# Optimization experiments

Hardware: AMD Instinct MI355X
Metric: run time of the kernel (lower is better)

## Reference

```python
import jax, jax.numpy as jnp
import numpy as np

B, T, F = 512, 1024, 8
H1, H2 = 70, 21   # '80k' config, bidirectional
D1, D2 = 30, 20


def _u(key, shape, fan):
    s = 1.0 / np.sqrt(fan)
    return jax.random.uniform(key, shape, jnp.float32, -s, s)


def setup_inputs() -> dict:
    key = jax.random.key(0)
    ks = iter(jax.random.split(key, 32))
    inp = {"x": jax.random.normal(next(ks), (B, T, F), jnp.float32)}
    # LSTM layer 1 (input F -> H1), forward and backward directions; torch gate order i,f,g,o
    for d in ("f", "b"):
        inp[f"w_ih1_{d}"] = _u(next(ks), (4 * H1, F), H1)
        inp[f"w_hh1_{d}"] = _u(next(ks), (4 * H1, H1), H1)
        inp[f"b_ih1_{d}"] = _u(next(ks), (4 * H1,), H1)
        inp[f"b_hh1_{d}"] = _u(next(ks), (4 * H1,), H1)
    # LSTM layer 2 (input 2*H1 -> H2)
    for d in ("f", "b"):
        inp[f"w_ih2_{d}"] = _u(next(ks), (4 * H2, 2 * H1), H2)
        inp[f"w_hh2_{d}"] = _u(next(ks), (4 * H2, H2), H2)
        inp[f"b_ih2_{d}"] = _u(next(ks), (4 * H2,), H2)
        inp[f"b_hh2_{d}"] = _u(next(ks), (4 * H2,), H2)
    # Dense head: 2*H2 -> D1 -> D2 -> 1
    inp["d1_w"] = _u(next(ks), (D1, 2 * H2), 2 * H2)
    inp["d1_b"] = _u(next(ks), (D1,), 2 * H2)
    inp["d2_w"] = _u(next(ks), (D2, D1), D1)
    inp["d2_b"] = _u(next(ks), (D2,), D1)
    inp["out_w"] = _u(next(ks), (1, D2), D2)
    inp["out_b"] = _u(next(ks), (1,), D2)
    return inp


def _lstm_dir(x, w_ih, w_hh, b_ih, b_hh, reverse):
    # x: [B, T, Fin]; torch LSTM gate order: i, f, g, o
    if reverse:
        x = x[:, ::-1]
    H = w_hh.shape[1]
    pre = jnp.einsum('btf,gf->btg', x, w_ih) + b_ih + b_hh  # [B, T, 4H]
    pre_t = jnp.moveaxis(pre, 1, 0)                          # [T, B, 4H]

    def step(carry, p):
        h, c = carry
        g = p + h @ w_hh.T
        i, f, gg, o = jnp.split(g, 4, axis=-1)
        c = jax.nn.sigmoid(f) * c + jax.nn.sigmoid(i) * jnp.tanh(gg)
        h = jax.nn.sigmoid(o) * jnp.tanh(c)
        return (h, c), h

    init = (jnp.zeros((x.shape[0], H), x.dtype), jnp.zeros((x.shape[0], H), x.dtype))
    _, hs = jax.lax.scan(step, init, pre_t)
    hs = jnp.moveaxis(hs, 0, 1)  # [B, T, H]
    if reverse:
        hs = hs[:, ::-1]
    return hs


def _bilstm(x, wf, uf, bif, bhf, wb, ub, bib, bhb):
    return jnp.concatenate([
        _lstm_dir(x, wf, uf, bif, bhf, reverse=False),
        _lstm_dir(x, wb, ub, bib, bhb, reverse=True),
    ], axis=-1)


def reference(x,
              w_ih1_f, w_hh1_f, b_ih1_f, b_hh1_f,
              w_ih1_b, w_hh1_b, b_ih1_b, b_hh1_b,
              w_ih2_f, w_hh2_f, b_ih2_f, b_hh2_f,
              w_ih2_b, w_hh2_b, b_ih2_b, b_hh2_b,
              d1_w, d1_b, d2_w, d2_b, out_w, out_b):
    h = _bilstm(x, w_ih1_f, w_hh1_f, b_ih1_f, b_hh1_f,
                w_ih1_b, w_hh1_b, b_ih1_b, b_hh1_b)   # [B, T, 2*H1]
    h = _bilstm(h, w_ih2_f, w_hh2_f, b_ih2_f, b_hh2_f,
                w_ih2_b, w_hh2_b, b_ih2_b, b_hh2_b)   # [B, T, 2*H2]
    h = jax.nn.relu(h @ d1_w.T + d1_b)
    h = jax.nn.relu(h @ d2_w.T + d2_b)
    return h @ out_w.T + out_b                          # [B, T, 1]
```

## Files before the change

### kernel.cpp

```cpp
#include <hip/hip_runtime.h>


typedef _Float16 v2f16 __attribute__((ext_vector_type(2)));
typedef _Float16 v4h   __attribute__((ext_vector_type(4)));
typedef _Float16 v8h   __attribute__((ext_vector_type(8)));
typedef float    f32x4 __attribute__((ext_vector_type(4)));

__device__ __forceinline__ float fdot2(v2f16 a, v2f16 b, float c) {
  return __builtin_amdgcn_fdot2(a, b, c, false);
}
#if __has_builtin(__builtin_amdgcn_rcpf)
__device__ __forceinline__ float rcpf(float x) { return __builtin_amdgcn_rcpf(x); }
#else
__device__ __forceinline__ float rcpf(float x) { return 1.f / x; }
#endif
__device__ __forceinline__ float ex2(float v) {
#if __has_builtin(__builtin_amdgcn_exp2f)
  return __builtin_amdgcn_exp2f(v);
#else
  return __expf(v * 0.6931471805599453f);
#endif
}

__device__ __forceinline__ void lds_barrier() {
  asm volatile("s_waitcnt lgkmcnt(0)" ::: "memory");
  __builtin_amdgcn_s_barrier();
  __builtin_amdgcn_sched_barrier(0);
}

#define O_W1M  0u
#define O_WP2  110592u
#define O_W2M  118656u
#define O_BIAS 177792u
#define O_DATA 178496u

__global__ void pack_kernel(const float* __restrict__ wihf, const float* __restrict__ whhf,
                            const float* __restrict__ wihb, const float* __restrict__ whhb,
                            const float* __restrict__ b1if, const float* __restrict__ b1hf,
                            const float* __restrict__ b1ib, const float* __restrict__ b1hb,
                            const float* __restrict__ wih2f, const float* __restrict__ wih2b,
                            const float* __restrict__ whh2f, const float* __restrict__ whh2b,
                            const float* __restrict__ bif, const float* __restrict__ bhf,
                            const float* __restrict__ bib, const float* __restrict__ bhb,
                            char* __restrict__ ws) {
  _Float16* w1m = (_Float16*)(ws + O_W1M);
  _Float16* wp2 = (_Float16*)(ws + O_WP2);
  _Float16* w2m = (_Float16*)(ws + O_W2M);
  float* biasc = (float*)(ws + O_BIAS);
  int idx = blockIdx.x * 256 + threadIdx.x;
  if (idx < 55296) {
    int d = idx / 27648, rem = idx % 27648, rp = rem / 96, k = rem % 96;
    int u = rp >> 2, g = rp & 3;
    const float* wih = d ? wihb : wihf;
    const float* whh = d ? whhb : whhf;
    const float* bi = d ? b1ib : b1if;
    const float* bh = d ? b1hb : b1hf;
    float v = 0.f;
    if (u < 70) {
      int src = g * 70 + u;
      float scale = (g == 2) ? 2.8853900817779268f : 1.4426950408889634f;
      if (k < 8) v = wih[src * 8 + k] * scale;
      else if (k < 78) v = whh[src * 70 + (k - 8)] * scale;
      else if (k == 78) v = (bi[src] + bh[src]) * scale;
    }
    w1m[idx] = (_Float16)v;
  } else if (idx < 59328) {
    int j = idx - 55296;
    int d = j / 2016, rem = j % 2016, r = rem / 24, k = rem % 24;
    const float* whh = d ? whh2b : whh2f;
    wp2[j] = (_Float16)((k < 21) ? whh[r * 21 + k] : 0.f);
  } else if (idx < 88896) {
    int j = idx - 59328;
    int n = j / 168, k = j % 168;
    float v = 0.f;
    if (k < 140) {
      if (n < 84) v = wih2f[n * 140 + k];
      else if (n < 168) v = wih2b[(n - 84) * 140 + k];
    }
    w2m[j] = (_Float16)v;
  } else if (idx < 89072) {
    int n = idx - 88896;
    float v = 0.f;
    if (n < 84) v = bif[n] + bhf[n];
    else if (n < 168) v = bib[n - 84] + bhb[n - 84];
    biasc[n] = v;
  }
}

__global__ __launch_bounds__(768) void lstm1_kernel(
    const float* __restrict__ x,
    const _Float16* __restrict__ w1m,
    _Float16* __restrict__ h1, int b0, int nb) {
  __shared__ __align__(16) _Float16 km[2][16][104];
  const int tid = threadIdx.x;
  const int w = tid >> 6, lane = tid & 63;
  const int q = lane >> 4, bc = lane & 15;
  const int d = blockIdx.y;
  const int blg = blockIdx.x * 16;
  const int gb0 = b0 + blg;

  for (int i = tid; i < 2 * 16 * 104; i += 768) ((_Float16*)km)[i] = (_Float16)0.f;

  int nt, T0;
  if (w < 4)       { nt = 1; T0 = w; }
  else if (w < 10) { nt = 2; T0 = 4 + 2 * (w - 4); }
  else             { nt = 1; T0 = 16 + (w - 10); }

  v8h af[2][3];
#pragma unroll
  for (int i = 0; i < 2; ++i) {
    if (i < nt) {
      int T = T0 + i;
#pragma unroll
      for (int kc = 0; kc < 3; ++kc)
        af[i][kc] = *(const v8h*)&w1m[(size_t)(d * 288 + T * 16 + bc) * 96 + kc * 32 + q * 8];
    }
  }

  __syncthreads();

  if (tid < 16) {
    km[0][tid][78] = (_Float16)1.f;
    km[1][tid][78] = (_Float16)1.f;
  }
  if (tid < 32) {
    int b = tid >> 1, half = tid & 1;
    int t0 = d ? 1023 : 0;
    float4 xv = *(const float4*)&x[((size_t)(gb0 + b) * 1024 + t0) * 8 + half * 4];
    v4h xh; xh[0] = (_Float16)xv.x; xh[1] = (_Float16)xv.y;
    xh[2] = (_Float16)xv.z; xh[3] = (_Float16)xv.w;
    *(v4h*)&km[0][b][half * 4] = xh;
  }
  float c0 = 0.f, c1 = 0.f;
  __syncthreads();

#pragma unroll 1
  for (int s = 0; s < 1024; ++s) {
    const int cur = s & 1, nxt = cur ^ 1;
    float4 xv;
    const bool xl = (tid < 32) && (s < 1023);
    if (xl) {
      int tn = d ? (1022 - s) : (s + 1);
      xv = *(const float4*)&x[((size_t)(gb0 + (tid >> 1)) * 1024 + tn) * 8 + (tid & 1) * 4];
    }
    v8h bf0 = *(const v8h*)&km[cur][bc][q * 8];
    v8h bf1 = *(const v8h*)&km[cur][bc][32 + q * 8];
    v8h bf2 = *(const v8h*)&km[cur][bc][64 + q * 8];
    f32x4 z4 = (f32x4){0.f, 0.f, 0.f, 0.f};
    f32x4 A0 = __builtin_amdgcn_mfma_f32_16x16x32_f16(af[0][0], bf0, z4, 0, 0, 0);
    f32x4 A1 = z4;
    if (nt == 2) A1 = __builtin_amdgcn_mfma_f32_16x16x32_f16(af[1][0], bf0, z4, 0, 0, 0);
    A0 = __builtin_amdgcn_mfma_f32_16x16x32_f16(af[0][1], bf1, A0, 0, 0, 0);
    if (nt == 2) A1 = __builtin_amdgcn_mfma_f32_16x16x32_f16(af[1][1], bf1, A1, 0, 0, 0);
    A0 = __builtin_amdgcn_mfma_f32_16x16x32_f16(af[0][2], bf2, A0, 0, 0, 0);
    if (nt == 2) A1 = __builtin_amdgcn_mfma_f32_16x16x32_f16(af[1][2], bf2, A1, 0, 0, 0);
    const int te = d ? (1023 - s) : s;
    const size_t rowb = ((size_t)te * nb + blg + bc) * 176 + d * 70;

#define GATE(Ai, ci, U)                                                      \
    {                                                                        \
      float ei = ex2(-Ai[0]);                                                \
      float ef = ex2(-Ai[1]);                                                \
      float eg = ex2(-Ai[2]);                                                \
      float eo = ex2(-Ai[3]);                                                \
      float si = rcpf(1.f + ei);                                             \
      float sf = rcpf(1.f + ef);                                             \
      float tg = fmaf(2.f, rcpf(1.f + eg), -1.f);                            \
      float so = rcpf(1.f + eo);                                             \
      ci = fmaf(sf, ci, si * tg);                                            \
      float ec = ex2(ci * -2.8853900817779268f);                             \
      float hv = so * fmaf(2.f, rcpf(1.f + ec), -1.f);                       \
      if ((U) < 70) {                                                        \
        _Float16 hh = (_Float16)hv;                                          \
        km[nxt][bc][8 + (U)] = hh;                                           \
        h1[rowb + (U)] = hh;                                                 \
      }                                                                      \
    }
    GATE(A0, c0, T0 * 4 + q)
    if (nt == 2) GATE(A1, c1, (T0 + 1) * 4 + q)
#undef GATE
    if (xl) {
      v4h xh; xh[0] = (_Float16)xv.x; xh[1] = (_Float16)xv.y;
      xh[2] = (_Float16)xv.z; xh[3] = (_Float16)xv.w;
      *(v4h*)&km[nxt][tid >> 1][(tid & 1) * 4] = xh;
    }
    lds_barrier();
  }
}

__global__ __launch_bounds__(256) void pre2_kernel(
    _Float16* __restrict__ h1, const char* __restrict__ ws) {
  const _Float16* w2m = (const _Float16*)(ws + O_W2M);
  const float* biasc = (const float*)(ws + O_BIAS);
  __shared__ _Float16 Al[64][184];
  __shared__ float Bl[176];
  const int tid = threadIdx.x;
  const int r0 = blockIdx.x * 64;
#pragma unroll
  for (int i = 0; i < 6; ++i) {
    int cid = i * 256 + tid;
    if (cid < 1408) {
      int row = cid / 22, ch = cid % 22;
      *(v8h*)&Al[row][ch * 8] = *(const v8h*)&h1[(size_t)(r0 + row) * 176 + ch * 8];
    }
  }
  if (tid < 176) Bl[tid] = biasc[tid];
  __syncthreads();

  const int wv = tid >> 6, lane = tid & 63;
  const int ml = lane & 15, kq = lane >> 4;
  v8h af[5];
#pragma unroll
  for (int k = 0; k < 4; ++k)
    af[k] = *(const v8h*)&Al[wv * 16 + ml][k * 32 + kq * 8];
  {
    v8h a4 = *(const v8h*)&Al[wv * 16 + ml][128 + kq * 8];
    if (kq >= 2) {
#pragma unroll
      for (int j = 0; j < 8; ++j) a4[j] = (_Float16)0.f;
    } else if (kq == 1) {
#pragma unroll
      for (int j = 4; j < 8; ++j) a4[j] = (_Float16)0.f;
    }
    af[4] = a4;
  }

  const v8h* wg = (const v8h*)w2m;
  f32x4 acc[11];
#pragma unroll
  for (int ct = 0; ct < 11; ++ct) acc[ct] = (f32x4){0.f, 0.f, 0.f, 0.f};

  v8h bc[5], bn[5];
#pragma unroll
  for (int k = 0; k < 5; ++k) bn[k] = wg[(size_t)ml * 21 + k * 4 + kq];
#pragma unroll
  for (int ct = 0; ct < 11; ++ct) {
#pragma unroll
    for (int k = 0; k < 5; ++k) bc[k] = bn[k];
    if (ct < 10) {
#pragma unroll
      for (int k = 0; k < 5; ++k) bn[k] = wg[(size_t)((ct + 1) * 16 + ml) * 21 + k * 4 + kq];
    }
#pragma unroll
    for (int k = 0; k < 5; ++k)
      acc[ct] = __builtin_amdgcn_mfma_f32_16x16x32_f16(af[k], bc[k], acc[ct], 0, 0, 0);
  }
  __syncthreads();
#pragma unroll
  for (int ct = 0; ct < 11; ++ct) {
#pragma unroll
    for (int r = 0; r < 4; ++r) {
      int row = wv * 16 + kq * 4 + r, col = ct * 16 + ml;
      Al[row][col] = (_Float16)(acc[ct][r] + Bl[col]);
    }
  }
  __syncthreads();
#pragma unroll
  for (int i = 0; i < 6; ++i) {
    int cid = i * 256 + tid;
    if (cid < 1408) {
      int row = cid / 22, ch = cid % 22;
      *(v8h*)&h1[(size_t)(r0 + row) * 176 + ch * 8] = *(const v8h*)&Al[row][ch * 8];
    }
  }
}

__global__ __launch_bounds__(64) void lstm2_kernel(
    const _Float16* __restrict__ pre2, const _Float16* __restrict__ wp2,
    _Float16* __restrict__ h2, int nb) {
  __shared__ __align__(16) _Float16 kv[2][32];
  const int lane = threadIdx.x;
  const int bl = blockIdx.x;
  const int d = blockIdx.y;
  const int u = lane >> 1, p = lane & 1;
  const bool active = lane < 42;

  ((_Float16*)kv)[lane] = (_Float16)0.f;

  v2f16 w0[12], w1[12];
  if (active) {
    const v8h* wr0 = (const v8h*)&wp2[(d * 84 + (2 * p) * 21 + u) * 24];
    const v8h* wr1 = (const v8h*)&wp2[(d * 84 + (2 * p + 1) * 21 + u) * 24];
#pragma unroll
    for (int ch = 0; ch < 3; ++ch) {
      v8h a = wr0[ch], b = wr1[ch];
#pragma unroll
      for (int q = 0; q < 4; ++q) {
        v2f16 t0; t0[0] = a[2 * q]; t0[1] = a[2 * q + 1]; w0[ch * 4 + q] = t0;
        v2f16 t1; t1[0] = b[2 * q]; t1[1] = b[2 * q + 1]; w1[ch * 4 + q] = t1;
      }
    }
  }
  const int col0 = d * 84 + (2 * p) * 21 + u;
  const int col1 = col0 + 21;
  const ptrdiff_t dlt = (ptrdiff_t)(d ? -nb : nb) * 176;
  const _Float16* pp = pre2 + ((size_t)(d ? 1023 : 0) * (size_t)nb + bl) * 176;

  _Float16 pa0 = pp[col0],            pa1 = pp[col1];
  _Float16 pb0 = (pp + dlt)[col0],    pb1 = (pp + dlt)[col1];
  _Float16 pc0 = (pp + 2*dlt)[col0],  pc1 = (pp + 2*dlt)[col1];
  _Float16 pd0 = (pp + 3*dlt)[col0],  pd1 = (pp + 3*dlt)[col1];
  const _Float16* pf = pp + 4 * dlt;

  const float esc0 = p ? -2.f : -1.f;
  const float ym0  = p ?  2.f :  1.f;
  const float ya0  = p ? -1.f :  0.f;
  float cc = 0.f;
  int s = 0;

#define L2STEP(P0, P1)                                                      \
  {                                                                         \
    const int cur = s & 1, nxt = cur ^ 1;                                   \
    float A0v = (float)P0, A1v = (float)P1;                                 \
    const float4* kp = (const float4*)&kv[cur][0];                          \
    float4 q0 = kp[0], q1 = kp[1], q2 = kp[2];                              \
    float x0 = A0v, x1 = 0.f, x2 = 0.f, x3 = 0.f;                           \
    float z0 = A1v, z1 = 0.f, z2 = 0.f, z3 = 0.f;                           \
    x0 = fdot2(__builtin_bit_cast(v2f16, q0.x), w0[0], x0);                 \
    x1 = fdot2(__builtin_bit_cast(v2f16, q0.y), w0[1], x1);                 \
    x2 = fdot2(__builtin_bit_cast(v2f16, q0.z), w0[2], x2);                 \
    x3 = fdot2(__builtin_bit_cast(v2f16, q0.w), w0[3], x3);                 \
    x0 = fdot2(__builtin_bit_cast(v2f16, q1.x), w0[4], x0);                 \
    x1 = fdot2(__builtin_bit_cast(v2f16, q1.y), w0[5], x1);                 \
    x2 = fdot2(__builtin_bit_cast(v2f16, q1.z), w0[6], x2);                 \
    x3 = fdot2(__builtin_bit_cast(v2f16, q1.w), w0[7], x3);                 \
    x0 = fdot2(__builtin_bit_cast(v2f16, q2.x), w0[8], x0);                 \
    x1 = fdot2(__builtin_bit_cast(v2f16, q2.y), w0[9], x1);                 \
    x2 = fdot2(__builtin_bit_cast(v2f16, q2.z), w0[10], x2);                \
    x3 = fdot2(__builtin_bit_cast(v2f16, q2.w), w0[11], x3);                \
    z0 = fdot2(__builtin_bit_cast(v2f16, q0.x), w1[0], z0);                 \
    z1 = fdot2(__builtin_bit_cast(v2f16, q0.y), w1[1], z1);                 \
    z2 = fdot2(__builtin_bit_cast(v2f16, q0.z), w1[2], z2);                 \
    z3 = fdot2(__builtin_bit_cast(v2f16, q0.w), w1[3], z3);                 \
    z0 = fdot2(__builtin_bit_cast(v2f16, q1.x), w1[4], z0);                 \
    z1 = fdot2(__builtin_bit_cast(v2f16, q1.y), w1[5], z1);                 \
    z2 = fdot2(__builtin_bit_cast(v2f16, q1.z), w1[6], z2);                 \
    z3 = fdot2(__builtin_bit_cast(v2f16, q1.w), w1[7], z3);                 \
    z0 = fdot2(__builtin_bit_cast(v2f16, q2.x), w1[8], z0);                 \
    z1 = fdot2(__builtin_bit_cast(v2f16, q2.y), w1[9], z1);                 \
    z2 = fdot2(__builtin_bit_cast(v2f16, q2.z), w1[10], z2);                \
    z3 = fdot2(__builtin_bit_cast(v2f16, q2.w), w1[11], z3);                \
    float A = (x0 + x1) + (x2 + x3), Bv = (z0 + z1) + (z2 + z3);            \
    float Y0 = fmaf(ym0, rcpf(1.f + __expf(A * esc0)), ya0);                \
    float Y1 = rcpf(1.f + __expf(-Bv));                                     \
    float Zs = __shfl_xor(Y0, 1);                                           \
    float Ws = __shfl_xor(Y1, 1);                                           \
    float ai = p ? Zs : Y0;                                                 \
    float af = p ? Ws : Y1;                                                 \
    float ag = p ? Y0 : Zs;                                                 \
    float ao = p ? Y1 : Ws;                                                 \
    cc = fmaf(af, cc, ai * ag);                                             \
    float tc = fmaf(2.f, rcpf(1.f + __expf(-2.f * cc)), -1.f);              \
    float hv = ao * tc;                                                     \
    if (active && p == 0) {                                                 \
      _Float16 hh = (_Float16)hv;                                           \
      int te = d ? (1023 - s) : s;                                          \
      kv[nxt][u] = hh;                                                      \
      h2[((size_t)te * nb + bl) * 48 + d * 21 + u] = hh;                    \
    }                                                                       \
    if (s < 1020) { P0 = pf[col0]; P1 = pf[col1]; }                         \
    pf += dlt;                                                              \
    ++s;                                                                    \
  }

#pragma unroll 1
  for (int it = 0; it < 256; ++it) {
    L2STEP(pa0, pa1)
    L2STEP(pb0, pb1)
    L2STEP(pc0, pc1)
    L2STEP(pd0, pd1)
  }
#undef L2STEP
}

__global__ __launch_bounds__(256) void head_kernel(
    const _Float16* __restrict__ h2,
    const float* __restrict__ d1w, const float* __restrict__ d1b,
    const float* __restrict__ d2w, const float* __restrict__ d2b,
    const float* __restrict__ ow, const float* __restrict__ ob,
    float* __restrict__ out, int b0, int lognb) {
  int n = blockIdx.x * 256 + threadIdx.x;
  int t = n >> lognb, bl = n & ((1 << lognb) - 1);
  const v8h* hp = (const v8h*)&h2[(size_t)n * 48];
  float in[48];
#pragma unroll
  for (int i = 0; i < 6; ++i) {
    v8h hc = hp[i];
#pragma unroll
    for (int j = 0; j < 8; ++j) in[i * 8 + j] = (float)hc[j];
  }
  float a1[30];
#pragma unroll
  for (int cc = 0; cc < 30; ++cc) {
    float a = d1b[cc];
#pragma unroll
    for (int k = 0; k < 42; ++k) a += in[k] * d1w[cc * 42 + k];
    a1[cc] = fmaxf(a, 0.f);
  }
  float a2[20];
#pragma unroll
  for (int cc = 0; cc < 20; ++cc) {
    float a = d2b[cc];
#pragma unroll
    for (int k = 0; k < 30; ++k) a += a1[k] * d2w[cc * 30 + k];
    a2[cc] = fmaxf(a, 0.f);
  }
  float o = ob[0];
#pragma unroll
  for (int k = 0; k < 20; ++k) o += a2[k] * ow[k];
  out[(size_t)(b0 + bl) * 1024 + t] = o;
}

extern "C" void kernel_launch(void* const* d_in, const int* in_sizes, int n_in,
                              void* d_out, int out_size, void* d_ws, size_t ws_size,
                              hipStream_t stream) {
  const float* x = (const float*)d_in[0];
  const float* wih1f = (const float*)d_in[1];
  const float* whh1f = (const float*)d_in[2];
  const float* bih1f = (const float*)d_in[3];
  const float* bhh1f = (const float*)d_in[4];
  const float* wih1b = (const float*)d_in[5];
  const float* whh1b = (const float*)d_in[6];
  const float* bih1b = (const float*)d_in[7];
  const float* bhh1b = (const float*)d_in[8];
  const float* wih2f = (const float*)d_in[9];
  const float* whh2f = (const float*)d_in[10];
  const float* bih2f = (const float*)d_in[11];
  const float* bhh2f = (const float*)d_in[12];
  const float* wih2b = (const float*)d_in[13];
  const float* whh2b = (const float*)d_in[14];
  const float* bih2b = (const float*)d_in[15];
  const float* bhh2b = (const float*)d_in[16];
  const float* d1w = (const float*)d_in[17];
  const float* d1b = (const float*)d_in[18];
  const float* d2w = (const float*)d_in[19];
  const float* d2b = (const float*)d_in[20];
  const float* ow = (const float*)d_in[21];
  const float* ob = (const float*)d_in[22];
  float* out = (float*)d_out;
  char* wsb = (char*)d_ws;

  const int cands[6] = {1, 2, 4, 8, 16, 32};
  int nslice = 32;
  for (int i = 0; i < 6; ++i) {
    size_t rows = (size_t)(512 / cands[i]) * 1024;
    if (O_DATA + rows * 448 <= ws_size) { nslice = cands[i]; break; }
  }
  const int nb = 512 / nslice;
  int lognb = 0; while ((1 << lognb) < nb) ++lognb;
  const size_t rows = (size_t)nb * 1024;

  _Float16* w1m = (_Float16*)(wsb + O_W1M);
  _Float16* wp2 = (_Float16*)(wsb + O_WP2);
  _Float16* h1  = (_Float16*)(wsb + O_DATA);
  _Float16* h2  = (_Float16*)(wsb + O_DATA + rows * 352);

  pack_kernel<<<348, 256, 0, stream>>>(wih1f, whh1f, wih1b, whh1b,
                                       bih1f, bhh1f, bih1b, bhh1b,
                                       wih2f, wih2b, whh2f, whh2b,
                                       bih2f, bhh2f, bih2b, bhh2b, wsb);

  for (int s = 0; s < nslice; ++s) {
    const int b0 = s * nb;
    lstm1_kernel<<<dim3(nb / 16, 2), 768, 0, stream>>>(x, w1m, h1, b0, nb);
    pre2_kernel<<<nb * 16, 256, 0, stream>>>(h1, wsb);
    lstm2_kernel<<<dim3(nb, 2), 64, 0, stream>>>(h1, wp2, h2, nb);
    head_kernel<<<nb * 4, 256, 0, stream>>>(h2, d1w, d1b, d2w, d2b, ow, ob,
                                            out, b0, lognb);
  }
}
```

Baseline: 1.383 ms.

## Use MFMA for layer-2 LSTM recurrence and rebalance layer-1 waves

Layer 2's recurrence changes from per-sequence fdot2 work (one 64-lane block per batch element) to 16-batch tiles computed with 16x16x32 f16 MFMA. The packed weights and bias are reordered into interleaved gate order and pre-scaled by log2e, so the gate math matches layer 1's exp2 form. Layer 1 drops from 12 to 8 waves, with each wave now handling two or three gate tiles, which reduces barrier participants. The trade-off is that lstm2 now pays an LDS barrier every step and launches far fewer blocks, so latency per step matters more.

After: 1.528 ms. +10.4%, slower.

```diff
diff --git a/kernel.cpp b/kernel.cpp
--- a/kernel.cpp
+++ b/kernel.cpp
@@ -6,9 +6,6 @@
 typedef _Float16 v8h   __attribute__((ext_vector_type(8)));
 typedef float    f32x4 __attribute__((ext_vector_type(4)));
 
-__device__ __forceinline__ float fdot2(v2f16 a, v2f16 b, float c) {
-  return __builtin_amdgcn_fdot2(a, b, c, false);
-}
 #if __has_builtin(__builtin_amdgcn_rcpf)
 __device__ __forceinline__ float rcpf(float x) { return __builtin_amdgcn_rcpf(x); }
 #else
@@ -28,11 +25,14 @@
   __builtin_amdgcn_sched_barrier(0);
 }
 
+#define LOG2E  1.4426950408889634f
+#define LOG2E2 2.8853900817779268f
+
 #define O_W1M  0u
-#define O_WP2  110592u
-#define O_W2M  118656u
-#define O_BIAS 177792u
-#define O_DATA 178496u
+#define O_W2HM 110592u
+#define O_W2M  122880u
+#define O_BIAS 182016u
+#define O_DATA 182720u
 
 __global__ void pack_kernel(const float* __restrict__ wihf, const float* __restrict__ whhf,
                             const float* __restrict__ wihb, const float* __restrict__ whhb,
@@ -43,9 +43,9 @@
                             const float* __restrict__ bif, const float* __restrict__ bhf,
                             const float* __restrict__ bib, const float* __restrict__ bhb,
                             char* __restrict__ ws) {
-  _Float16* w1m = (_Float16*)(ws + O_W1M);
-  _Float16* wp2 = (_Float16*)(ws + O_WP2);
-  _Float16* w2m = (_Float16*)(ws + O_W2M);
+  _Float16* w1m  = (_Float16*)(ws + O_W1M);
+  _Float16* w2hm = (_Float16*)(ws + O_W2HM);
+  _Float16* w2m  = (_Float16*)(ws + O_W2M);
   float* biasc = (float*)(ws + O_BIAS);
   int idx = blockIdx.x * 256 + threadIdx.x;
   if (idx < 55296) {
@@ -58,36 +58,49 @@
     float v = 0.f;
     if (u < 70) {
       int src = g * 70 + u;
-      float scale = (g == 2) ? 2.8853900817779268f : 1.4426950408889634f;
+      float scale = (g == 2) ? LOG2E2 : LOG2E;
       if (k < 8) v = wih[src * 8 + k] * scale;
       else if (k < 78) v = whh[src * 70 + (k - 8)] * scale;
       else if (k == 78) v = (bi[src] + bh[src]) * scale;
     }
     w1m[idx] = (_Float16)v;
-  } else if (idx < 59328) {
+  } else if (idx < 61440) {
     int j = idx - 55296;
-    int d = j / 2016, rem = j % 2016, r = rem / 24, k = rem % 24;
+    int d = j / 3072, rem = j % 3072, rp = rem / 32, k = rem % 32;
+    int u = rp >> 2, g = rp & 3;
     const float* whh = d ? whh2b : whh2f;
-    wp2[j] = (_Float16)((k < 21) ? whh[r * 21 + k] : 0.f);
-  } else if (idx < 88896) {
-    int j = idx - 59328;
+    float v = 0.f;
+    if (u < 21 && k < 21) {
+      float scale = (g == 2) ? LOG2E2 : LOG2E;
+      v = whh[(g * 21 + u) * 21 + k] * scale;
+    }
+    w2hm[j] = (_Float16)v;
+  } else if (idx < 91008) {
+    int j = idx - 61440;
     int n = j / 168, k = j % 168;
     float v = 0.f;
-    if (k < 140) {
-      if (n < 84) v = wih2f[n * 140 + k];
-      else if (n < 168) v = wih2b[(n - 84) * 140 + k];
+    if (n < 168 && k < 140) {
+      int d = n / 84, m = n % 84, u = m >> 2, g = m & 3;
+      const float* wih = d ? wih2b : wih2f;
+      float scale = (g == 2) ? LOG2E2 : LOG2E;
+      v = wih[(g * 21 + u) * 140 + k] * scale;
     }
     w2m[j] = (_Float16)v;
-  } else if (idx < 89072) {
-    int n = idx - 88896;
+  } else if (idx < 91184) {
+    int n = idx - 91008;
     float v = 0.f;
-    if (n < 84) v = bif[n] + bhf[n];
-    else if (n < 168) v = bib[n - 84] + bhb[n - 84];
+    if (n < 168) {
+      int d = n / 84, m = n % 84, u = m >> 2, g = m & 3;
+      const float* bi = d ? bib : bif;
+      const float* bh = d ? bhb : bhf;
+      float scale = (g == 2) ? LOG2E2 : LOG2E;
+      v = (bi[g * 21 + u] + bh[g * 21 + u]) * scale;
+    }
     biasc[n] = v;
   }
 }
 
-__global__ __launch_bounds__(768) void lstm1_kernel(
+__global__ __launch_bounds__(512) void lstm1_kernel(
     const float* __restrict__ x,
     const _Float16* __restrict__ w1m,
     _Float16* __restrict__ h1, int b0, int nb) {
@@ -99,22 +112,21 @@
   const int blg = blockIdx.x * 16;
   const int gb0 = b0 + blg;
 
-  for (int i = tid; i < 2 * 16 * 104; i += 768) ((_Float16*)km)[i] = (_Float16)0.f;
-
-  int nt, T0;
-  if (w < 4)       { nt = 1; T0 = w; }
-  else if (w < 10) { nt = 2; T0 = 4 + 2 * (w - 4); }
-  else             { nt = 1; T0 = 16 + (w - 10); }
-
-  v8h af[2][3];
-#pragma unroll
-  for (int i = 0; i < 2; ++i) {
-    if (i < nt) {
-      int T = T0 + i;
-#pragma unroll
-      for (int kc = 0; kc < 3; ++kc)
-        af[i][kc] = *(const v8h*)&w1m[(size_t)(d * 288 + T * 16 + bc) * 96 + kc * 32 + q * 8];
-    }
+  for (int i = tid; i < 2 * 16 * 104; i += 512) ((_Float16*)km)[i] = (_Float16)0.f;
+
+  const bool three = (w < 2);
+  const int T0 = three ? 3 * w : 6 + 2 * (w - 2);
+
+  v8h af[3][3];
+#pragma unroll
+  for (int kc = 0; kc < 3; ++kc) {
+    af[0][kc] = *(const v8h*)&w1m[(size_t)(d * 288 + T0 * 16 + bc) * 96 + kc * 32 + q * 8];
+    af[1][kc] = *(const v8h*)&w1m[(size_t)(d * 288 + (T0 + 1) * 16 + bc) * 96 + kc * 32 + q * 8];
+  }
+  if (three) {
+#pragma unroll
+    for (int kc = 0; kc < 3; ++kc)
+      af[2][kc] = *(const v8h*)&w1m[(size_t)(d * 288 + (T0 + 2) * 16 + bc) * 96 + kc * 32 + q * 8];
   }
 
   __syncthreads();
@@ -123,37 +135,41 @@
     km[0][tid][78] = (_Float16)1.f;
     km[1][tid][78] = (_Float16)1.f;
   }
-  if (tid < 32) {
-    int b = tid >> 1, half = tid & 1;
+  const bool xlane = (tid >= 448 && tid < 480);
+  if (xlane) {
+    int b = (tid - 448) >> 1, half = (tid - 448) & 1;
     int t0 = d ? 1023 : 0;
     float4 xv = *(const float4*)&x[((size_t)(gb0 + b) * 1024 + t0) * 8 + half * 4];
     v4h xh; xh[0] = (_Float16)xv.x; xh[1] = (_Float16)xv.y;
     xh[2] = (_Float16)xv.z; xh[3] = (_Float16)xv.w;
     *(v4h*)&km[0][b][half * 4] = xh;
   }
-  float c0 = 0.f, c1 = 0.f;
+  float c0 = 0.f, c1 = 0.f, c2 = 0.f;
   __syncthreads();
 
 #pragma unroll 1
   for (int s = 0; s < 1024; ++s) {
     const int cur = s & 1, nxt = cur ^ 1;
     float4 xv;
-    const bool xl = (tid < 32) && (s < 1023);
+    const bool xl = xlane && (s < 1023);
     if (xl) {
       int tn = d ? (1022 - s) : (s + 1);
-      xv = *(const float4*)&x[((size_t)(gb0 + (tid >> 1)) * 1024 + tn) * 8 + (tid & 1) * 4];
+      xv = *(const float4*)&x[((size_t)(gb0 + ((tid - 448) >> 1)) * 1024 + tn) * 8 + ((tid - 448) & 1) * 4];
     }
     v8h bf0 = *(const v8h*)&km[cur][bc][q * 8];
     v8h bf1 = *(const v8h*)&km[cur][bc][32 + q * 8];
     v8h bf2 = *(const v8h*)&km[cur][bc][64 + q * 8];
     f32x4 z4 = (f32x4){0.f, 0.f, 0.f, 0.f};
     f32x4 A0 = __builtin_amdgcn_mfma_f32_16x16x32_f16(af[0][0], bf0, z4, 0, 0, 0);
-    f32x4 A1 = z4;
-    if (nt == 2) A1 = __builtin_amdgcn_mfma_f32_16x16x32_f16(af[1][0], bf0, z4, 0, 0, 0);
+    f32x4 A1 = __builtin_amdgcn_mfma_f32_16x16x32_f16(af[1][0], bf0, z4, 0, 0, 0);
+    f32x4 A2 = z4;
+    if (three) A2 = __builtin_amdgcn_mfma_f32_16x16x32_f16(af[2][0], bf0, z4, 0, 0, 0);
     A0 = __builtin_amdgcn_mfma_f32_16x16x32_f16(af[0][1], bf1, A0, 0, 0, 0);
-    if (nt == 2) A1 = __builtin_amdgcn_mfma_f32_16x16x32_f16(af[1][1], bf1, A1, 0, 0, 0);
+    A1 = __builtin_amdgcn_mfma_f32_16x16x32_f16(af[1][1], bf1, A1, 0, 0, 0);
+    if (three) A2 = __builtin_amdgcn_mfma_f32_16x16x32_f16(af[2][1], bf1, A2, 0, 0, 0);
     A0 = __builtin_amdgcn_mfma_f32_16x16x32_f16(af[0][2], bf2, A0, 0, 0, 0);
-    if (nt == 2) A1 = __builtin_amdgcn_mfma_f32_16x16x32_f16(af[1][2], bf2, A1, 0, 0, 0);
+    A1 = __builtin_amdgcn_mfma_f32_16x16x32_f16(af[1][2], bf2, A1, 0, 0, 0);
+    if (three) A2 = __builtin_amdgcn_mfma_f32_16x16x32_f16(af[2][2], bf2, A2, 0, 0, 0);
     const int te = d ? (1023 - s) : s;
     const size_t rowb = ((size_t)te * nb + blg + bc) * 176 + d * 70;
 
@@ -168,7 +184,7 @@
       float tg = fmaf(2.f, rcpf(1.f + eg), -1.f);                            \
       float so = rcpf(1.f + eo);                                             \
       ci = fmaf(sf, ci, si * tg);                                            \
-      float ec = ex2(ci * -2.8853900817779268f);                             \
+      float ec = ex2(ci * -LOG2E2);                                          \
       float hv = so * fmaf(2.f, rcpf(1.f + ec), -1.f);                       \
       if ((U) < 70) {                                                        \
         _Float16 hh = (_Float16)hv;                                          \
@@ -177,12 +193,13 @@
       }                                                                      \
     }
     GATE(A0, c0, T0 * 4 + q)
-    if (nt == 2) GATE(A1, c1, (T0 + 1) * 4 + q)
+    GATE(A1, c1, (T0 + 1) * 4 + q)
+    if (three) GATE(A2, c2, (T0 + 2) * 4 + q)
 #undef GATE
     if (xl) {
       v4h xh; xh[0] = (_Float16)xv.x; xh[1] = (_Float16)xv.y;
       xh[2] = (_Float16)xv.z; xh[3] = (_Float16)xv.w;
-      *(v4h*)&km[nxt][tid >> 1][(tid & 1) * 4] = xh;
+      *(v4h*)&km[nxt][(tid - 448) >> 1][((tid - 448) & 1) * 4] = xh;
     }
     lds_barrier();
   }
@@ -265,112 +282,105 @@
   }
 }
 
-__global__ __launch_bounds__(64) void lstm2_kernel(
-    const _Float16* __restrict__ pre2, const _Float16* __restrict__ wp2,
+__global__ __launch_bounds__(256) void lstm2_kernel(
+    const _Float16* __restrict__ pre2, const _Float16* __restrict__ w2hm,
     _Float16* __restrict__ h2, int nb) {
-  __shared__ __align__(16) _Float16 kv[2][32];
-  const int lane = threadIdx.x;
-  const int bl = blockIdx.x;
+  __shared__ __align__(16) _Float16 kv[2][16][40];
+  const int tid = threadIdx.x;
+  const int w = tid >> 6, lane = tid & 63;
+  const int q = lane >> 4, bc = lane & 15;
   const int d = blockIdx.y;
-  const int u = lane >> 1, p = lane & 1;
-  const bool active = lane < 42;
-
-  ((_Float16*)kv)[lane] = (_Float16)0.f;
-
-  v2f16 w0[12], w1[12];
-  if (active) {
-    const v8h* wr0 = (const v8h*)&wp2[(d * 84 + (2 * p) * 21 + u) * 24];
-    const v8h* wr1 = (const v8h*)&wp2[(d * 84 + (2 * p + 1) * 21 + u) * 24];
-#pragma unroll
-    for (int ch = 0; ch < 3; ++ch) {
-      v8h a = wr0[ch], b = wr1[ch];
-#pragma unroll
-      for (int q = 0; q < 4; ++q) {
-        v2f16 t0; t0[0] = a[2 * q]; t0[1] = a[2 * q + 1]; w0[ch * 4 + q] = t0;
-        v2f16 t1; t1[0] = b[2 * q]; t1[1] = b[2 * q + 1]; w1[ch * 4 + q] = t1;
-      }
-    }
-  }
-  const int col0 = d * 84 + (2 * p) * 21 + u;
-  const int col1 = col0 + 21;
+  const int blg = blockIdx.x * 16;
+
+  for (int i = tid; i < 2 * 16 * 40; i += 256) ((_Float16*)kv)[i] = (_Float16)0.f;
+
+  const bool two = (w < 2);
+  const int T0 = two ? 2 * w : 4 + (w - 2);
+  const int U0 = T0 * 4 + q;
+  const int U1 = (T0 + 1) * 4 + q;
+
+  v8h af0 = *(const v8h*)&w2hm[(size_t)(d * 96 + T0 * 16 + bc) * 32 + q * 8];
+  v8h af1 = af0;
+  if (two) af1 = *(const v8h*)&w2hm[(size_t)(d * 96 + (T0 + 1) * 16 + bc) * 32 + q * 8];
+
+  const int cb0 = d * 84 + 4 * (U0 < 21 ? U0 : 20);
+  const int cb1 = d * 84 + 4 * (U1 < 21 ? U1 : 20);
   const ptrdiff_t dlt = (ptrdiff_t)(d ? -nb : nb) * 176;
-  const _Float16* pp = pre2 + ((size_t)(d ? 1023 : 0) * (size_t)nb + bl) * 176;
-
-  _Float16 pa0 = pp[col0],            pa1 = pp[col1];
-  _Float16 pb0 = (pp + dlt)[col0],    pb1 = (pp + dlt)[col1];
-  _Float16 pc0 = (pp + 2*dlt)[col0],  pc1 = (pp + 2*dlt)[col1];
-  _Float16 pd0 = (pp + 3*dlt)[col0],  pd1 = (pp + 3*dlt)[col1];
+  const _Float16* pp = pre2 + ((size_t)(d ? 1023 : 0) * nb + blg + bc) * 176;
+
+  v4h pA0 = *(const v4h*)(pp + cb0);
+  v4h pB0 = *(const v4h*)(pp + dlt + cb0);
+  v4h pC0 = *(const v4h*)(pp + 2 * dlt + cb0);
+  v4h pD0 = *(const v4h*)(pp + 3 * dlt + cb0);
+  v4h pA1 = pA0, pB1 = pB0, pC1 = pC0, pD1 = pD0;
+  if (two) {
+    pA1 = *(const v4h*)(pp + cb1);
+    pB1 = *(const v4h*)(pp + dlt + cb1);
+    pC1 = *(const v4h*)(pp + 2 * dlt + cb1);
+    pD1 = *(const v4h*)(pp + 3 * dlt + cb1);
+  }
   const _Float16* pf = pp + 4 * dlt;
 
-  const float esc0 = p ? -2.f : -1.f;
-  const float ym0  = p ?  2.f :  1.f;
-  const float ya0  = p ? -1.f :  0.f;
-  float cc = 0.f;
+  float cs0 = 0.f, cs1 = 0.f;
   int s = 0;
-
-#define L2STEP(P0, P1)                                                      \
-  {                                                                         \
-    const int cur = s & 1, nxt = cur ^ 1;                                   \
-    float A0v = (float)P0, A1v = (float)P1;                                 \
-    const float4* kp = (const float4*)&kv[cur][0];                          \
-    float4 q0 = kp[0], q1 = kp[1], q2 = kp[2];                              \
-    float x0 = A0v, x1 = 0.f, x2 = 0.f, x3 = 0.f;                           \
-    float z0 = A1v, z1 = 0.f, z2 = 0.f, z3 = 0.f;                           \
-    x0 = fdot2(__builtin_bit_cast(v2f16, q0.x), w0[0], x0);                 \
-    x1 = fdot2(__builtin_bit_cast(v2f16, q0.y), w0[1], x1);                 \
-    x2 = fdot2(__builtin_bit_cast(v2f16, q0.z), w0[2], x2);                 \
-    x3 = fdot2(__builtin_bit_cast(v2f16, q0.w), w0[3], x3);                 \
-    x0 = fdot2(__builtin_bit_cast(v2f16, q1.x), w0[4], x0);                 \
-    x1 = fdot2(__builtin_bit_cast(v2f16, q1.y), w0[5], x1);                 \
-    x2 = fdot2(__builtin_bit_cast(v2f16, q1.z), w0[6], x2);                 \
-    x3 = fdot2(__builtin_bit_cast(v2f16, q1.w), w0[7], x3);                 \
-    x0 = fdot2(__builtin_bit_cast(v2f16, q2.x), w0[8], x0);                 \
-    x1 = fdot2(__builtin_bit_cast(v2f16, q2.y), w0[9], x1);                 \
-    x2 = fdot2(__builtin_bit_cast(v2f16, q2.z), w0[10], x2);                \
-    x3 = fdot2(__builtin_bit_cast(v2f16, q2.w), w0[11], x3);                \
-    z0 = fdot2(__builtin_bit_cast(v2f16, q0.x), w1[0], z0);                 \
-    z1 = fdot2(__builtin_bit_cast(v2f16, q0.y), w1[1], z1);                 \
-    z2 = fdot2(__builtin_bit_cast(v2f16, q0.z), w1[2], z2);                 \
-    z3 = fdot2(__builtin_bit_cast(v2f16, q0.w), w1[3], z3);                 \
-    z0 = fdot2(__builtin_bit_cast(v2f16, q1.x), w1[4], z0);                 \
-    z1 = fdot2(__builtin_bit_cast(v2f16, q1.y), w1[5], z1);                 \
-    z2 = fdot2(__builtin_bit_cast(v2f16, q1.z), w1[6], z2);                 \
-    z3 = fdot2(__builtin_bit_cast(v2f16, q1.w), w1[7], z3);                 \
-    z0 = fdot2(__builtin_bit_cast(v2f16, q2.x), w1[8], z0);                 \
-    z1 = fdot2(__builtin_bit_cast(v2f16, q2.y), w1[9], z1);                 \
-    z2 = fdot2(__builtin_bit_cast(v2f16, q2.z), w1[10], z2);                \
-    z3 = fdot2(__builtin_bit_cast(v2f16, q2.w), w1[11], z3);                \
-    float A = (x0 + x1) + (x2 + x3), Bv = (z0 + z1) + (z2 + z3);            \
-    float Y0 = fmaf(ym0, rcpf(1.f + __expf(A * esc0)), ya0);                \
-    float Y1 = rcpf(1.f + __expf(-Bv));                                     \
-    float Zs = __shfl_xor(Y0, 1);                                           \
-    float Ws = __shfl_xor(Y1, 1);                                           \
-    float ai = p ? Zs : Y0;                                                 \
-    float af = p ? Ws : Y1;                                                 \
-    float ag = p ? Y0 : Zs;                                                 \
-    float ao = p ? Y1 : Ws;                                                 \
-    cc = fmaf(af, cc, ai * ag);                                             \
-    float tc = fmaf(2.f, rcpf(1.f + __expf(-2.f * cc)), -1.f);              \
-    float hv = ao * tc;                                                     \
-    if (active && p == 0) {                                                 \
-      _Float16 hh = (_Float16)hv;                                           \
-      int te = d ? (1023 - s) : s;                                          \
-      kv[nxt][u] = hh;                                                      \
-      h2[((size_t)te * nb + bl) * 48 + d * 21 + u] = hh;                    \
-    }                                                                       \
-    if (s < 1020) { P0 = pf[col0]; P1 = pf[col1]; }                         \
-    pf += dlt;                                                              \
-    ++s;                                                                    \
+  __syncthreads();
+
+#define GATE2(Ai, ci, U)                                                    \
+    {                                                                       \
+      float ei = ex2(-Ai[0]);                                               \
+      float ef = ex2(-Ai[1]);                                               \
+      float eg = ex2(-Ai[2]);                                                \
+      float eo = ex2(-Ai[3]);                                               \
+      float si = rcpf(1.f + ei);                                            \
+      float sf = rcpf(1.f + ef);                                            \
+      float tg = fmaf(2.f, rcpf(1.f + eg), -1.f);                           \
+      float so = rcpf(1.f + eo);                                            \
+      ci = fmaf(sf, ci, si * tg);                                           \
+      float ec = ex2(ci * -LOG2E2);                                         \
+      float hv = so * fmaf(2.f, rcpf(1.f + ec), -1.f);                      \
+      if ((U) < 21) {                                                       \
+        _Float16 hh = (_Float16)hv;                                         \
+        kv[nxt][bc][U] = hh;                                                \
+        h2[rowb + d * 21 + (U)] = hh;                                       \
+      }                                                                     \
+    }
+
+#define L2STEP(P0, P1)                                                     \
+  {                                                                        \
+    const int cur = s & 1, nxt = cur ^ 1;                                  \
+    v8h bf = *(const v8h*)&kv[cur][bc][q * 8];                             \
+    f32x4 ci0;                                                             \
+    ci0[0] = (float)P0[0]; ci0[1] = (float)P0[1];                          \
+    ci0[2] = (float)P0[2]; ci0[3] = (float)P0[3];                          \
+    f32x4 A0 = __builtin_amdgcn_mfma_f32_16x16x32_f16(af0, bf, ci0, 0, 0, 0); \
+    const int te = d ? (1023 - s) : s;                                     \
+    const size_t rowb = ((size_t)te * nb + blg + bc) * 48;                 \
+    GATE2(A0, cs0, U0)                                                     \
+    if (two) {                                                             \
+      f32x4 ci1;                                                           \
+      ci1[0] = (float)P1[0]; ci1[1] = (float)P1[1];                        \
+      ci1[2] = (float)P1[2]; ci1[3] = (float)P1[3];                        \
+      f32x4 A1 = __builtin_amdgcn_mfma_f32_16x16x32_f16(af1, bf, ci1, 0, 0, 0); \
+      GATE2(A1, cs1, U1)                                                   \
+    }                                                                      \
+    if (s < 1020) {                                                        \
+      P0 = *(const v4h*)(pf + cb0);                                        \
+      if (two) P1 = *(const v4h*)(pf + cb1);                               \
+    }                                                                      \
+    pf += dlt;                                                             \
+    ++s;                                                                   \
+    lds_barrier();                                                         \
   }
 
 #pragma unroll 1
   for (int it = 0; it < 256; ++it) {
-    L2STEP(pa0, pa1)
-    L2STEP(pb0, pb1)
-    L2STEP(pc0, pc1)
-    L2STEP(pd0, pd1)
+    L2STEP(pA0, pA1)
+    L2STEP(pB0, pB1)
+    L2STEP(pC0, pC1)
+    L2STEP(pD0, pD1)
   }
 #undef L2STEP
+#undef GATE2
 }
 
 __global__ __launch_bounds__(256) void head_kernel(
@@ -450,21 +460,21 @@
   int lognb = 0; while ((1 << lognb) < nb) ++lognb;
   const size_t rows = (size_t)nb * 1024;
 
-  _Float16* w1m = (_Float16*)(wsb + O_W1M);
-  _Float16* wp2 = (_Float16*)(wsb + O_WP2);
-  _Float16* h1  = (_Float16*)(wsb + O_DATA);
-  _Float16* h2  = (_Float16*)(wsb + O_DATA + rows * 352);
-
-  pack_kernel<<<348, 256, 0, stream>>>(wih1f, whh1f, wih1b, whh1b,
+  _Float16* w1m  = (_Float16*)(wsb + O_W1M);
+  _Float16* w2hm = (_Float16*)(wsb + O_W2HM);
+  _Float16* h1   = (_Float16*)(wsb + O_DATA);
+  _Float16* h2   = (_Float16*)(wsb + O_DATA + rows * 352);
+
+  pack_kernel<<<357, 256, 0, stream>>>(wih1f, whh1f, wih1b, whh1b,
                                        bih1f, bhh1f, bih1b, bhh1b,
                                        wih2f, wih2b, whh2f, whh2b,
                                        bih2f, bhh2f, bih2b, bhh2b, wsb);
 
   for (int s = 0; s < nslice; ++s) {
     const int b0 = s * nb;
-    lstm1_kernel<<<dim3(nb / 16, 2), 768, 0, stream>>>(x, w1m, h1, b0, nb);
+    lstm1_kernel<<<dim3(nb / 16, 2), 512, 0, stream>>>(x, w1m, h1, b0, nb);
     pre2_kernel<<<nb * 16, 256, 0, stream>>>(h1, wsb);
-    lstm2_kernel<<<dim3(nb, 2), 64, 0, stream>>>(h1, wp2, h2, nb);
+    lstm2_kernel<<<dim3(nb / 16, 2), 256, 0, stream>>>(h1, w2hm, h2, nb);
     head_kernel<<<nb * 4, 256, 0, stream>>>(h2, d1w, d1b, d2w, d2b, ow, ob,
                                             out, b0, lognb);
   }
```
